# Kernel optimization log

Hardware: AMD Instinct MI355X
Metric: run time of the kernel (lower is better)

## Reference

```python
import jax, jax.numpy as jnp
import numpy as np
from jax import lax

NUM_CLASSES = 13
H, W = 120, 160
INLIER_THRESHOLD = 0.9
LABEL_THRESHOLD = 500
THRESHOLD_VOTE = 10.0
THRESHOLD_PERCENTAGE = 0.02
SKIP_PIXELS = 16


def setup_inputs() -> dict:
    key = jax.random.key(0)
    k0, k1, k2, k3 = jax.random.split(key, 4)
    labels = jax.random.randint(k0, (1, H, W), 0, NUM_CLASSES, dtype=jnp.int32)
    masks = jnp.ones((1, H, W), jnp.int32)
    vertex_pred = jax.random.normal(k1, (1, 3 * NUM_CLASSES, H, W), jnp.float32)
    extents = jax.random.uniform(k2, (NUM_CLASSES, 3), jnp.float32, 0.05, 0.3)
    poses = jax.random.normal(k3, (1, 13), jnp.float32)
    # flattened 3x3 intrinsics K: fx=meta[0], px=meta[2], fy=meta[4], py=meta[5]
    meta_data = jnp.array([[500.0, 0.0, W / 2.0, 0.0, 500.0, H / 2.0, 0.0, 0.0, 1.0]], jnp.float32)
    return {"labels": labels, "masks": masks, "vertex_pred": vertex_pred,
            "extents": extents, "poses": poses, "meta_data": meta_data}


def _hough_forward(labels, masks, vertex_pred, extents, poses, meta_data):
    B = labels.shape[0]
    HW = H * W
    ys, xs = jnp.meshgrid(jnp.arange(H, dtype=jnp.float32),
                          jnp.arange(W, dtype=jnp.float32), indexing="ij")
    coords_g = jnp.stack([xs.reshape(-1), ys.reshape(-1)], axis=1)  # [HW,2] center candidates
    samp = jnp.arange(0, HW, SKIP_PIXELS)                            # subsampled voting pixels
    coords_p = coords_g[samp]                                        # [P,2]

    def per_image(args):
        lab, msk, vp, meta = args
        lab_f = lab.reshape(-1)
        valid_pix = msk.reshape(-1) > 0
        fx, fy, pxc, pyc = meta[0], meta[4], meta[2], meta[5]

        def per_class(c):
            mask_full = (lab_f == c) & valid_pix            # [HW]
            num_label = jnp.sum(mask_full)
            labeled_p = mask_full[samp]                     # [P]
            vpc = lax.dynamic_slice_in_dim(vp, 3 * c, 3, axis=0)  # [3,H,W]
            dx = vpc[0].reshape(-1)[samp]
            dy = vpc[1].reshape(-1)[samp]
            dz_full = vpc[2].reshape(-1)
            dn = jnp.sqrt(dx * dx + dy * dy) + 1e-6
            dxn, dyn = dx / dn, dy / dn
            # displacement from each voting pixel to every candidate center: [P,HW]
            ddx = coords_g[None, :, 0] - coords_p[:, None, 0]
            ddy = coords_g[None, :, 1] - coords_p[:, None, 1]
            dist = jnp.sqrt(ddx * ddx + ddy * ddy)
            cosang = (ddx * dxn[:, None] + ddy * dyn[:, None]) / jnp.maximum(dist, 1e-6)
            inlier = (cosang > INLIER_THRESHOLD) & (dist > 0.0) & labeled_p[:, None]
            votes = jnp.sum(inlier.astype(jnp.float32), axis=0)  # [HW] Hough accumulator
            best = jnp.argmax(votes)
            vmax = votes[best]
            cx, cy = coords_g[best, 0], coords_g[best, 1]
            # depth: exp of mean predicted log-depth over this class's pixels
            msum = jnp.maximum(num_label.astype(jnp.float32), 1.0)
            z = jnp.exp(jnp.sum(dz_full * mask_full.astype(jnp.float32)) / msum)
            z = jnp.maximum(z, 1e-3)
            bw = extents[c, 0] * fx / z
            bh = extents[c, 1] * fy / z
            nsamp = jnp.maximum(jnp.sum(labeled_p).astype(jnp.float32), 1.0)
            valid = (vmax >= THRESHOLD_VOTE) & (num_label >= LABEL_THRESHOLD) & \
                    (vmax >= THRESHOLD_PERCENTAGE * nsamp)
            cf = c.astype(jnp.float32)
            box = jnp.stack([cf, cx - bw / 2, cy - bh / 2, cx + bw / 2, cy + bh / 2, vmax])
            tx = (cx - pxc) * z / fx
            ty = (cy - pyc) * z / fy
            one = jnp.ones_like(z)
            zero = jnp.zeros_like(z)
            pose = jnp.stack([one, zero, zero, zero, tx, ty, z])  # identity quat + translation
            onehot = (jnp.arange(4 * NUM_CLASSES) // 4 == c).astype(jnp.float32)
            weight = valid.astype(jnp.float32) * onehot
            target = jnp.zeros((4 * NUM_CLASSES,), jnp.float32)
            return box, pose, target, weight

        return lax.map(per_class, jnp.arange(1, NUM_CLASSES))

    boxes, poses_o, targets, weights = lax.map(per_image, (labels, masks, vertex_pred, meta_data))
    Cm1 = NUM_CLASSES - 1
    N = B * Cm1
    bidx = jnp.repeat(jnp.arange(B, dtype=jnp.float32), Cm1)[:, None]
    top_box = jnp.concatenate([bidx, boxes.reshape(N, 6)], axis=1)      # [N,7]
    top_pose = poses_o.reshape(N, 7)
    top_target = targets.reshape(N, 4 * NUM_CLASSES)
    top_weight = weights.reshape(N, 4 * NUM_CLASSES)
    top_domain = jnp.repeat(jnp.arange(B, dtype=jnp.int32), Cm1)
    return top_box, top_pose, top_target, top_weight, top_domain


def reference(labels, masks, vertex_pred, extents, poses, meta_data):
    return _hough_forward(labels, masks, vertex_pred, extents, poses, meta_data)
```

## Files before the change

### kernel.cpp

```cpp
#include <hip/hip_runtime.h>
#include <hip/hip_bf16.h>

#define NCLS 13
#define HH 120
#define WW 160
#define HWSZ (HH * WW)
#define PSAMP 1200
#define CM1 (NCLS - 1)
#define NBLK 75


__global__ void hough_prep(const int* __restrict__ labels,
                           const int* __restrict__ masks,
                           const float* __restrict__ vp,
                           float4* __restrict__ praw,
                           int* __restrict__ bcnt,
                           int* __restrict__ pcnt,
                           float* __restrict__ pdz,
                           int* __restrict__ best) {
    const int tid = threadIdx.x;
    const int b = blockIdx.x;
    const int i = b * 256 + tid;
    __shared__ int lcnt[CM1];
    if (tid < CM1) lcnt[tid] = 0;
    if (b == 0 && tid >= 64 && tid < 64 + CM1) best[tid - 64] = 0;
    __syncthreads();

    const int lab = labels[i];
    const bool valid = (lab > 0) && (masks[i] > 0);
    const int cls = valid ? lab - 1 : -1;
    float dz = 0.f;
    if (valid) dz = vp[(3 * lab + 2) * HWSZ + i];

    if (valid && ((tid & 15) == 0)) {
        float dx = vp[(3 * lab + 0) * HWSZ + i];
        float dy = vp[(3 * lab + 1) * HWSZ + i];
        float dn = __fadd_rn(
            __fsqrt_rn(__fadd_rn(__fmul_rn(dx, dx), __fmul_rn(dy, dy))), 1e-6f);
        int k = atomicAdd(&lcnt[cls], 1);
        praw[(cls * NBLK + b) * 16 + k] =
            make_float4((float)(i % WW), (float)(i / WW),
                        __fdiv_rn(dx, dn), __fdiv_rn(dy, dn));
    }

    __shared__ float s_dz[4][CM1];
    __shared__ int   s_ct[4][CM1];
    const int w = tid >> 6, lane = tid & 63;
    for (int c1 = 0; c1 < CM1; ++c1) {
        unsigned long long bl = __ballot(cls == c1);
        float v = (cls == c1) ? dz : 0.f;
        for (int off = 32; off > 0; off >>= 1) v += __shfl_xor(v, off);
        if (lane == 0) { s_ct[w][c1] = (int)__popcll(bl); s_dz[w][c1] = v; }
    }
    __syncthreads();
    if (tid < CM1) {
        bcnt[tid * NBLK + b] = lcnt[tid];
        pcnt[tid * NBLK + b] = s_ct[0][tid] + s_ct[1][tid] + s_ct[2][tid] + s_ct[3][tid];
        pdz [tid * NBLK + b] = ((s_dz[0][tid] + s_dz[1][tid]) + s_dz[2][tid]) + s_dz[3][tid];
    }
}

__global__ void hough_vote(const float4* __restrict__ praw,
                           const int* __restrict__ bcnt,
                           int* __restrict__ best) {
    const int c1 = blockIdx.y;
    const int g  = blockIdx.x * 256 + threadIdx.x;
    __shared__ float4 s[PSAMP];
    __shared__ int scnt[NBLK];
    __shared__ int soff[NBLK + 1];
    if (threadIdx.x < NBLK) scnt[threadIdx.x] = bcnt[c1 * NBLK + threadIdx.x];
    __syncthreads();
    if (threadIdx.x == 0) {
        int acc = 0;
        for (int b2 = 0; b2 < NBLK; ++b2) { soff[b2] = acc; acc += scnt[b2]; }
        soff[NBLK] = acc;
    }
    __syncthreads();
    for (int t = threadIdx.x; t < NBLK * 16; t += 256) {
        const int b2 = t >> 4, k = t & 15;
        if (k < scnt[b2]) s[soff[b2] + k] = praw[(c1 * NBLK + b2) * 16 + k];
    }
    const int n = soff[NBLK];
    __syncthreads();

    const float xg = (float)(g % WW);
    const float yg = (float)(g / WW);
    int v = 0;
    for (int j = 0; j < n; ++j) {
        float4 e = s[j];
        float ddx = __fsub_rn(xg, e.x);
        float ddy = __fsub_rn(yg, e.y);
        float d2  = __fadd_rn(__fmul_rn(ddx, ddx), __fmul_rn(ddy, ddy));
        float dist = __fsqrt_rn(d2);
        float t2 = __fadd_rn(__fmul_rn(ddx, e.z), __fmul_rn(ddy, e.w));
        float cosang = __fdiv_rn(t2, fmaxf(dist, 1e-6f));
        v += (cosang > 0.9f && dist > 0.0f) ? 1 : 0;
    }

    int key = (v << 15) | (19199 - g);
    for (int off = 32; off > 0; off >>= 1) {
        int o = __shfl_xor(key, off);
        key = key > o ? key : o;
    }
    __shared__ int wmax[4];
    if ((threadIdx.x & 63) == 0) wmax[threadIdx.x >> 6] = key;
    __syncthreads();
    if (threadIdx.x == 0) {
        int k01 = wmax[0] > wmax[1] ? wmax[0] : wmax[1];
        int k23 = wmax[2] > wmax[3] ? wmax[2] : wmax[3];
        atomicMax(&best[c1], k01 > k23 ? k01 : k23);
    }
}

__global__ void hough_out(const int* __restrict__ best,
                          const int* __restrict__ bcnt,
                          const int* __restrict__ pcnt,
                          const float* __restrict__ pdz,
                          const float* __restrict__ extents,
                          const float* __restrict__ meta,
                          float* __restrict__ out) {
    const int tid = threadIdx.x;
    float* top_box    = out;
    float* top_pose   = out + 84;
    float* top_target = out + 168;
    float* top_weight = out + 792;
    float* top_domain = out + 1416;

    for (int j = tid; j < 624; j += 256) top_target[j] = 0.f;
    if (tid >= 244) top_domain[tid - 244] = 0.f;

    if (tid < CM1) {
        const int c1 = tid, c = tid + 1;
        int nl = 0, ns = 0; float ds = 0.f;
        #pragma unroll
        for (int b = 0; b < NBLK; ++b) {
            nl += pcnt[c1 * NBLK + b];
            ns += bcnt[c1 * NBLK + b];
            ds += pdz [c1 * NBLK + b];
        }
        const int key = best[c1];
        const float vmax = (float)(key >> 15);
        const int bi = 19199 - (key & 32767);
        const float cx = (float)(bi % WW);
        const float cy = (float)(bi / WW);
        const float msum = fmaxf((float)nl, 1.0f);
        float z = expf(ds / msum);
        z = fmaxf(z, 1e-3f);
        const float fx = meta[0], fy = meta[4], pxc = meta[2], pyc = meta[5];
        const float bw = extents[c * 3 + 0] * fx / z;
        const float bh = extents[c * 3 + 1] * fy / z;
        const float nsamp = fmaxf((float)ns, 1.0f);
        const bool valid = (vmax >= 10.0f) && (nl >= 500) &&
                           (vmax >= 0.02f * nsamp);

        float* bx = top_box + c1 * 7;
        bx[0] = 0.0f;
        bx[1] = (float)c;
        bx[2] = cx - bw * 0.5f;
        bx[3] = cy - bh * 0.5f;
        bx[4] = cx + bw * 0.5f;
        bx[5] = cy + bh * 0.5f;
        bx[6] = vmax;

        const float tx = (cx - pxc) * z / fx;
        const float ty = (cy - pyc) * z / fy;
        float* ps = top_pose + c1 * 7;
        ps[0] = 1.f; ps[1] = 0.f; ps[2] = 0.f; ps[3] = 0.f;
        ps[4] = tx;  ps[5] = ty;  ps[6] = z;

        float* wt = top_weight + c1 * 52;
        const float wv = valid ? 1.0f : 0.0f;
        for (int j = 0; j < 52; ++j)
            wt[j] = ((j >> 2) == c) ? wv : 0.0f;
    }
}

extern "C" void kernel_launch(void* const* d_in, const int* in_sizes, int n_in,
                              void* d_out, int out_size, void* d_ws, size_t ws_size,
                              hipStream_t stream) {
    const int*   labels  = (const int*)d_in[0];
    const int*   masks   = (const int*)d_in[1];
    const float* vp      = (const float*)d_in[2];
    const float* extents = (const float*)d_in[3];
    const float* meta    = (const float*)d_in[5];
    float* out = (float*)d_out;

    char* ws = (char*)d_ws;
    float4* praw = (float4*)(ws + 0);
    int*    bcnt = (int*)   (ws + 230400);
    int*    pcnt = (int*)   (ws + 234000);
    float*  pdz  = (float*) (ws + 237600);
    int*    best = (int*)   (ws + 241200);

    hough_prep<<<dim3(NBLK), dim3(256), 0, stream>>>(labels, masks, vp,
                                                     praw, bcnt, pcnt, pdz, best);
    hough_vote<<<dim3(NBLK, CM1), dim3(256), 0, stream>>>(praw, bcnt, best);
    hough_out<<<dim3(1), dim3(256), 0, stream>>>(best, bcnt, pcnt, pdz,
                                                 extents, meta, out);
}
```

Baseline: 37.19 us.

## Fuse output kernel into vote kernel via last-block completion counter

Merges the final output kernel into the voting kernel. An atomic counter with thread fences lets the last finishing block compute the outputs, which removes one kernel launch. The serial prefix scan used to compact samples is replaced by a shared-memory atomic append. The per-class reduction in the output stage is parallelised across 16 lanes per class. Sample order now varies from run to run, but the vote count is an integer sum, so results should not change.

```diff
diff --git a/kernel.cpp b/kernel.cpp
--- a/kernel.cpp
+++ b/kernel.cpp
@@ -8,6 +8,7 @@
 #define PSAMP 1200
 #define CM1 (NCLS - 1)
 #define NBLK 75
+#define NVOTE (NBLK * CM1)
 
 
 __global__ void hough_prep(const int* __restrict__ labels,
@@ -17,13 +18,13 @@
                            int* __restrict__ bcnt,
                            int* __restrict__ pcnt,
                            float* __restrict__ pdz,
-                           int* __restrict__ best) {
+                           int* __restrict__ best13) {
     const int tid = threadIdx.x;
     const int b = blockIdx.x;
     const int i = b * 256 + tid;
     __shared__ int lcnt[CM1];
     if (tid < CM1) lcnt[tid] = 0;
-    if (b == 0 && tid >= 64 && tid < 64 + CM1) best[tid - 64] = 0;
+    if (b == 0 && tid < CM1 + 1) best13[tid] = 0;
     __syncthreads();
 
     const int lab = labels[i];
@@ -60,28 +61,34 @@
     }
 }
 
-__global__ void hough_vote(const float4* __restrict__ praw,
-                           const int* __restrict__ bcnt,
-                           int* __restrict__ best) {
+__global__ void hough_vote_out(const float4* __restrict__ praw,
+                               const int* __restrict__ bcnt,
+                               const int* __restrict__ pcnt,
+                               const float* __restrict__ pdz,
+                               const float* __restrict__ extents,
+                               const float* __restrict__ meta,
+                               int* __restrict__ best13,
+                               float* __restrict__ out) {
     const int c1 = blockIdx.y;
     const int g  = blockIdx.x * 256 + threadIdx.x;
+    const int tid = threadIdx.x;
     __shared__ float4 s[PSAMP];
     __shared__ int scnt[NBLK];
-    __shared__ int soff[NBLK + 1];
-    if (threadIdx.x < NBLK) scnt[threadIdx.x] = bcnt[c1 * NBLK + threadIdx.x];
-    __syncthreads();
-    if (threadIdx.x == 0) {
-        int acc = 0;
-        for (int b2 = 0; b2 < NBLK; ++b2) { soff[b2] = acc; acc += scnt[b2]; }
-        soff[NBLK] = acc;
-    }
-    __syncthreads();
-    for (int t = threadIdx.x; t < NBLK * 16; t += 256) {
+    __shared__ int s_n;
+    __shared__ int wmax[4];
+    __shared__ int is_last;
+    if (tid == 0) s_n = 0;
+    if (tid < NBLK) scnt[tid] = bcnt[c1 * NBLK + tid];
+    __syncthreads();
+    for (int t = tid; t < NBLK * 16; t += 256) {
         const int b2 = t >> 4, k = t & 15;
-        if (k < scnt[b2]) s[soff[b2] + k] = praw[(c1 * NBLK + b2) * 16 + k];
-    }
-    const int n = soff[NBLK];
-    __syncthreads();
+        if (k < scnt[b2]) {
+            int pos = atomicAdd(&s_n, 1);
+            s[pos] = praw[(c1 * NBLK + b2) * 16 + k];
+        }
+    }
+    __syncthreads();
+    const int n = s_n;
 
     const float xg = (float)(g % WW);
     const float yg = (float)(g / WW);
@@ -102,24 +109,20 @@
         int o = __shfl_xor(key, off);
         key = key > o ? key : o;
     }
-    __shared__ int wmax[4];
-    if ((threadIdx.x & 63) == 0) wmax[threadIdx.x >> 6] = key;
-    __syncthreads();
-    if (threadIdx.x == 0) {
+    if ((tid & 63) == 0) wmax[tid >> 6] = key;
+    __syncthreads();
+    if (tid == 0) {
         int k01 = wmax[0] > wmax[1] ? wmax[0] : wmax[1];
         int k23 = wmax[2] > wmax[3] ? wmax[2] : wmax[3];
-        atomicMax(&best[c1], k01 > k23 ? k01 : k23);
-    }
-}
-
-__global__ void hough_out(const int* __restrict__ best,
-                          const int* __restrict__ bcnt,
-                          const int* __restrict__ pcnt,
-                          const float* __restrict__ pdz,
-                          const float* __restrict__ extents,
-                          const float* __restrict__ meta,
-                          float* __restrict__ out) {
-    const int tid = threadIdx.x;
+        atomicMax(&best13[c1], k01 > k23 ? k01 : k23);
+        __threadfence();
+        int old = atomicAdd(&best13[CM1], 1);
+        is_last = (old == NVOTE - 1) ? 1 : 0;
+    }
+    __syncthreads();
+    if (!is_last) return;
+
+    __threadfence();
     float* top_box    = out;
     float* top_pose   = out + 84;
     float* top_target = out + 168;
@@ -129,18 +132,40 @@
     for (int j = tid; j < 624; j += 256) top_target[j] = 0.f;
     if (tid >= 244) top_domain[tid - 244] = 0.f;
 
+    __shared__ int   r_nl[CM1][16];
+    __shared__ int   r_ns[CM1][16];
+    __shared__ float r_dz[CM1][16];
+    if (tid < CM1 * 16) {
+        const int cc = tid >> 4, l = tid & 15;
+        int nl = 0, ns = 0; float ds = 0.f;
+        for (int b = l; b < NBLK; b += 16) {
+            nl += pcnt[cc * NBLK + b];
+            ns += bcnt[cc * NBLK + b];
+            ds += pdz [cc * NBLK + b];
+        }
+        r_nl[cc][l] = nl; r_ns[cc][l] = ns; r_dz[cc][l] = ds;
+    }
+    __syncthreads();
+    for (int st = 8; st > 0; st >>= 1) {
+        if (tid < CM1 * 16) {
+            const int cc = tid >> 4, l = tid & 15;
+            if (l < st) {
+                r_nl[cc][l] += r_nl[cc][l + st];
+                r_ns[cc][l] += r_ns[cc][l + st];
+                r_dz[cc][l] += r_dz[cc][l + st];
+            }
+        }
+        __syncthreads();
+    }
+
     if (tid < CM1) {
-        const int c1 = tid, c = tid + 1;
-        int nl = 0, ns = 0; float ds = 0.f;
-        #pragma unroll
-        for (int b = 0; b < NBLK; ++b) {
-            nl += pcnt[c1 * NBLK + b];
-            ns += bcnt[c1 * NBLK + b];
-            ds += pdz [c1 * NBLK + b];
-        }
-        const int key = best[c1];
-        const float vmax = (float)(key >> 15);
-        const int bi = 19199 - (key & 32767);
+        const int cc = tid, c = tid + 1;
+        const int nl = r_nl[cc][0];
+        const int ns = r_ns[cc][0];
+        const float ds = r_dz[cc][0];
+        const int key2 = atomicMax(&best13[cc], 0);
+        const float vmax = (float)(key2 >> 15);
+        const int bi = 19199 - (key2 & 32767);
         const float cx = (float)(bi % WW);
         const float cy = (float)(bi / WW);
         const float msum = fmaxf((float)nl, 1.0f);
@@ -153,7 +178,7 @@
         const bool valid = (vmax >= 10.0f) && (nl >= 500) &&
                            (vmax >= 0.02f * nsamp);
 
-        float* bx = top_box + c1 * 7;
+        float* bx = top_box + cc * 7;
         bx[0] = 0.0f;
         bx[1] = (float)c;
         bx[2] = cx - bw * 0.5f;
@@ -164,11 +189,11 @@
 
         const float tx = (cx - pxc) * z / fx;
         const float ty = (cy - pyc) * z / fy;
-        float* ps = top_pose + c1 * 7;
+        float* ps = top_pose + cc * 7;
         ps[0] = 1.f; ps[1] = 0.f; ps[2] = 0.f; ps[3] = 0.f;
         ps[4] = tx;  ps[5] = ty;  ps[6] = z;
 
-        float* wt = top_weight + c1 * 52;
+        float* wt = top_weight + cc * 52;
         const float wv = valid ? 1.0f : 0.0f;
         for (int j = 0; j < 52; ++j)
             wt[j] = ((j >> 2) == c) ? wv : 0.0f;
@@ -186,15 +211,14 @@
     float* out = (float*)d_out;
 
     char* ws = (char*)d_ws;
-    float4* praw = (float4*)(ws + 0);
-    int*    bcnt = (int*)   (ws + 230400);
-    int*    pcnt = (int*)   (ws + 234000);
-    float*  pdz  = (float*) (ws + 237600);
-    int*    best = (int*)   (ws + 241200);
+    float4* praw   = (float4*)(ws + 0);
+    int*    bcnt   = (int*)   (ws + 230400);
+    int*    pcnt   = (int*)   (ws + 234000);
+    float*  pdz    = (float*) (ws + 237600);
+    int*    best13 = (int*)   (ws + 241200);
 
     hough_prep<<<dim3(NBLK), dim3(256), 0, stream>>>(labels, masks, vp,
-                                                     praw, bcnt, pcnt, pdz, best);
-    hough_vote<<<dim3(NBLK, CM1), dim3(256), 0, stream>>>(praw, bcnt, best);
-    hough_out<<<dim3(1), dim3(256), 0, stream>>>(best, bcnt, pcnt, pdz,
-                                                 extents, meta, out);
+                                                     praw, bcnt, pcnt, pdz, best13);
+    hough_vote_out<<<dim3(NBLK, CM1), dim3(256), 0, stream>>>(
+        praw, bcnt, pcnt, pdz, extents, meta, best13, out);
 }
```

Result: slower. 41.94 us (+12.8%).
